# Performance work log

Hardware: AMD Instinct MI355X
Metric: run time of the kernel (lower is better)

## Reference

```python
import jax, jax.numpy as jnp
import numpy as np

SCALES = [2 ** i for i in range(11)]  # scales=10 -> [1,2,4,...,1024]


def _linear_upsample(x, N):
    """torch F.interpolate(mode='linear', align_corners=False) along last axis.
    x: (B, C, pn) -> (B, C, N)."""
    pn = x.shape[-1]
    scale = pn / N
    coords = (jnp.arange(N, dtype=x.dtype) + 0.5) * scale - 0.5
    coords = jnp.clip(coords, 0.0, pn - 1)
    i0 = jnp.floor(coords).astype(jnp.int32)
    i1 = jnp.minimum(i0 + 1, pn - 1)
    w = (coords - i0.astype(x.dtype))
    return x[..., i0] * (1.0 - w) + x[..., i1] * w


def setup_inputs() -> dict:
    key = jax.random.key(0)
    k1, k2 = jax.random.split(key)
    B, N, C, K = 32, 1024, 512, 4096
    f_BNC = jax.random.normal(k1, (B, N, C), dtype=jnp.float32)
    # torch init: uniform(-1/K, 1/K)
    codebook = (jax.random.uniform(k2, (K, C), dtype=jnp.float32) * 2.0 - 1.0) / K
    return {"f_BNC": f_BNC, "codebook": codebook}


def reference(f_BNC, codebook):
    f_BCN = jnp.transpose(f_BNC, (0, 2, 1))  # (B, C, N)
    B, C, N = f_BCN.shape
    f_ng = jax.lax.stop_gradient(f_BCN)      # f_no_grad
    f_rest = f_ng
    f_hat = jnp.zeros_like(f_ng)
    Wd = jax.lax.stop_gradient(codebook)     # embedding.weight.data for distances
    w_sq = jnp.sum(Wd * Wd, axis=1)          # (K,)
    SN = len(SCALES)
    commit = jnp.zeros((), dtype=f_BCN.dtype)
    qlat = jnp.zeros((), dtype=f_BCN.dtype)
    for pn in SCALES:
        # area downsample: exact block mean since N % pn == 0
        r = f_rest.reshape(B, C, pn, N // pn).mean(axis=-1)        # (B, C, pn)
        z = jnp.transpose(r, (0, 2, 1)).reshape(B * pn, C)          # (B*pn, C)
        d = jnp.sum(z * z, axis=1, keepdims=True) + w_sq - 2.0 * (z @ Wd.T)  # (B*pn, K)
        p = jax.nn.softmax(d, axis=-1)
        h = (p @ codebook).reshape(B, pn, C)                        # soft codebook lookup
        h = jnp.transpose(h, (0, 2, 1))                             # (B, C, pn)
        h = _linear_upsample(h, N)                                  # (B, C, N)
        f_hat = f_hat + h
        f_rest = f_rest - h
        commit = commit + 0.25 * jnp.mean((jax.lax.stop_gradient(f_hat) - f_BCN) ** 2)
        qlat = qlat + jnp.mean((f_hat - f_ng) ** 2)
    commit = commit / SN
    qlat = qlat / SN
    # straight-through estimator
    f_hat_st = jax.lax.stop_gradient(f_hat) - f_ng + f_BCN
    return jnp.transpose(f_hat_st, (0, 2, 1)), commit, qlat
```

## Files before the change

### kernel.cpp

```cpp
#include <hip/hip_runtime.h>
#include <hip/hip_bf16.h>

constexpr int B = 32, N = 1024, C = 512, K = 4096, SN = 11;
constexpr long BCN = (long)B * N * C;
constexpr int TKC = 128;
constexpr int NCH = K / TKC;
constexpr float PSCALE = 256.f;
constexpr int SCONE = 0x7f7f7f7f;

typedef __attribute__((ext_vector_type(4))) float f32x4;
typedef __attribute__((ext_vector_type(16))) float f32x16;
typedef __attribute__((ext_vector_type(8))) int i32x8;
typedef __attribute__((ext_vector_type(4))) int i32x4;
typedef unsigned int u32;
typedef unsigned long u64;

static __device__ __forceinline__ short f2bf(float x) {
  __hip_bfloat16 h = __float2bfloat16(x);
  short s;
  __builtin_memcpy(&s, &h, sizeof(s));
  return s;
}
static __device__ __forceinline__ float bf2f(short s) {
  u32 u = ((u32)(unsigned short)s) << 16;
  float f;
  __builtin_memcpy(&f, &u, 4);
  return f;
}
static __device__ __forceinline__ u32 pk4_fp8(float a, float b, float c, float d) {
  int r = __builtin_amdgcn_cvt_pk_fp8_f32(a, b, 0, false);
  r = __builtin_amdgcn_cvt_pk_fp8_f32(c, d, r, true);
  return (u32)r;
}
static __device__ __forceinline__ f32x16 zero16() {
  f32x16 z;
#pragma unroll
  for (int i = 0; i < 16; ++i) z[i] = 0.f;
  return z;
}

__global__ __launch_bounds__(256) void wsq_kernel(const float* __restrict__ W,
                                                  float* __restrict__ wsq) {
  __shared__ float red[256];
  int k = blockIdx.x;
  const float* row = W + (long)k * C;
  float s = 0.f;
  for (int c = threadIdx.x; c < C; c += 256) {
    float v = row[c];
    s += v * v;
  }
  red[threadIdx.x] = s;
  __syncthreads();
  for (int off = 128; off > 0; off >>= 1) {
    if (threadIdx.x < off) red[threadIdx.x] += red[threadIdx.x + off];
    __syncthreads();
  }
  if (threadIdx.x == 0) wsq[k] = red[0];
}

__global__ __launch_bounds__(256) void colsum_kernel(const float* __restrict__ W,
                                                     float* __restrict__ csum) {
  int ch = blockIdx.x;
  const float* base = W + (long)ch * TKC * C;
  float s0 = 0.f, s1 = 0.f;
  for (int k = 0; k < TKC; ++k) {
    s0 += base[(long)k * C + threadIdx.x];
    s1 += base[(long)k * C + threadIdx.x + 256];
  }
  csum[ch * C + threadIdx.x] = s0;
  csum[ch * C + threadIdx.x + 256] = s1;
}

__global__ __launch_bounds__(256) void prep_w(const float* __restrict__ W,
                                              unsigned char* __restrict__ WnA,
                                              unsigned char* __restrict__ WtB) {
  __shared__ __attribute__((aligned(16))) unsigned char tile[32 * 520];
  const int blk = blockIdx.x, tid = threadIdx.x;
  const float* src = W + (long)blk * 32 * C;
#pragma unroll
  for (int i = 0; i < 16; ++i) {
    int idx = tid + i * 256;
    float4 v = ((const float4*)src)[idx];
    int key = idx >> 7, c = (idx & 127) * 4;
    *(u32*)&tile[key * 520 + c] = pk4_fp8(v.x, v.y, v.z, v.w);
  }
  __syncthreads();
#pragma unroll
  for (int i = 0; i < 2; ++i) {
    int slot = tid + i * 256;
    int cc = slot >> 6, L = slot & 63;
    const unsigned char* sp = &tile[(L & 31) * 520 + cc * 64 + (L >> 5) * 32];
    u64* dst = (u64*)(WnA + ((long)(blk * 8 + cc) * 64 + L) * 32);
    dst[0] = *(const u64*)(sp);
    dst[1] = *(const u64*)(sp + 8);
    dst[2] = *(const u64*)(sp + 16);
    dst[3] = *(const u64*)(sp + 24);
  }
#pragma unroll
  for (int i = 0; i < 2; ++i) {
    int slot = tid + i * 256;
    int c2 = slot >> 5, rho = slot & 31;
    union { unsigned char v[32]; u64 q[4]; } t;
#pragma unroll
    for (int j = 0; j < 32; ++j) t.v[j] = tile[j * 520 + c2 * 32 + rho];
    u64* dst = (u64*)(WtB + ((long)((blk >> 1) * 16 + c2) * 64 + (blk & 1) * 32 + rho) * 32);
    dst[0] = t.q[0]; dst[1] = t.q[1]; dst[2] = t.q[2]; dst[3] = t.q[3];
  }
}

__global__ __launch_bounds__(256) void init_f(const float* __restrict__ f,
                                              short* __restrict__ fbf,
                                              float* __restrict__ zpart) {
  int b = blockIdx.x >> 5;
  int n0 = (blockIdx.x & 31) * 32 + (threadIdx.x >> 7) * 16;
  int c4 = threadIdx.x & 127;
  float ax = 0, ay = 0, az = 0, aw = 0;
  for (int j = 0; j < 16; ++j) {
    long e = ((long)b * N + n0 + j) * 128 + c4;
    float4 v = ((const float4*)f)[e];
    short4 o = {f2bf(v.x), f2bf(v.y), f2bf(v.z), f2bf(v.w)};
    ((short4*)fbf)[e] = o;
    ax += v.x; ay += v.y; az += v.z; aw += v.w;
  }
  float4 zp = {ax, ay, az, aw};
  ((float4*)zpart)[((long)b * 64 + (n0 >> 4)) * 128 + c4] = zp;
}

__global__ __launch_bounds__(256) void reduce_zpart(const float* __restrict__ zpart,
                                                    unsigned char* __restrict__ zq, int pn) {
  long idx = (long)blockIdx.x * 256 + threadIdx.x;
  long tot = (long)B * pn * 128;
  if (idx >= tot) return;
  int c4 = (int)(idx & 127);
  long row = idx >> 7;
  int b = (int)(row / pn), j = (int)(row % pn);
  int r = 64 / pn;
  float ax = 0, ay = 0, az = 0, aw = 0;
  for (int i = 0; i < r; ++i) {
    float4 v = ((const float4*)zpart)[((long)b * 64 + j * r + i) * 128 + c4];
    ax += v.x; ay += v.y; az += v.z; aw += v.w;
  }
  float inv = (float)pn / (float)N;
  *(u32*)&zq[row * C + c4 * 4] = pk4_fp8(ax * inv, ay * inv, az * inv, aw * inv);
}

__global__ __launch_bounds__(256, 2) void flash_mfma(
    const unsigned char* __restrict__ zq, const unsigned char* __restrict__ WnA,
    const unsigned char* __restrict__ WtB, const float* __restrict__ wsq,
    const float* __restrict__ csum, short* __restrict__ hb,
    float* __restrict__ lpart, int M, int KS) {
  __shared__ __attribute__((aligned(16))) unsigned char ZS[16 * 2048];
  __shared__ __attribute__((aligned(16))) unsigned char PS[2][4 * 2048];
  const int tid = threadIdx.x;
  const int w = tid >> 6, lane = tid & 63;
  const int rho = lane & 31, hi = lane >> 5;
  const long row0 = (long)blockIdx.x * 64;
  const int nc = NCH / KS, ch0 = blockIdx.y * nc;

#pragma unroll
  for (int i = 0; i < 4; ++i) {
    int u = i * 4 + w, zt = u >> 3, cc = u & 7;
    long row = row0 + zt * 32 + rho;
    u64 v0 = 0, v1 = 0, v2 = 0, v3 = 0;
    if (row < M) {
      const u64* sp = (const u64*)(zq + row * C + cc * 64 + hi * 32);
      v0 = sp[0]; v1 = sp[1]; v2 = sp[2]; v3 = sp[3];
    }
    u64* dp = (u64*)(ZS + u * 2048 + lane * 32);
    dp[0] = v0; dp[1] = v1; dp[2] = v2; dp[3] = v3;
  }
  f32x16 hacc[2][4];
#pragma unroll
  for (int zt = 0; zt < 2; ++zt)
#pragma unroll
    for (int ct = 0; ct < 4; ++ct) hacc[zt][ct] = zero16();
  float lreg[2] = {0.f, 0.f};
  float cs[4] = {0.f, 0.f, 0.f, 0.f};
  __syncthreads();

#pragma unroll 1
  for (int ci = 0; ci < nc; ++ci) {
    const int ch = ch0 + ci;
#pragma unroll
    for (int ct = 0; ct < 4; ++ct) cs[ct] += csum[ch * C + w * 128 + ct * 32 + rho];
    f32x16 s[2];
    s[0] = zero16();
    s[1] = zero16();
    const unsigned char* wa = WnA + ((long)(ch * 4 + w) * 8) * 2048 + lane * 32;
    const unsigned char* zb = ZS + lane * 32;
#pragma unroll
    for (int cc = 0; cc < 8; ++cc) {
      i32x8 a = *(const i32x8*)(wa + cc * 2048);
      i32x8 b0 = *(const i32x8*)(zb + cc * 2048);
      i32x8 b1 = *(const i32x8*)(zb + (8 + cc) * 2048);
      s[0] = __builtin_amdgcn_mfma_scale_f32_32x32x64_f8f6f4(a, b0, s[0], 0, 0, 0, SCONE, 0, SCONE);
      s[1] = __builtin_amdgcn_mfma_scale_f32_32x32x64_f8f6f4(a, b1, s[1], 0, 0, 0, SCONE, 0, SCONE);
    }
    const float* wsb = wsq + ch * TKC + w * 32 + hi * 4;
    float wv[16];
#pragma unroll
    for (int g = 0; g < 4; ++g) {
      float4 t = *(const float4*)(wsb + 8 * g);
      wv[4 * g + 0] = t.x; wv[4 * g + 1] = t.y; wv[4 * g + 2] = t.z; wv[4 * g + 3] = t.w;
    }
    unsigned char* Pun = PS[ci & 1] + (w >> 1) * 2048;
    const int pbase = (w & 1) * 1024 + rho * 32 + hi * 4;
#pragma unroll
    for (int zt = 0; zt < 2; ++zt) {
      float sum = 0.f, pv[16];
#pragma unroll
      for (int r = 0; r < 16; ++r) {
        float e = __expf(wv[r] - 2.f * s[zt][r]);
        sum += e;
        pv[r] = PSCALE * e - PSCALE;
      }
      lreg[zt] += sum;
#pragma unroll
      for (int g = 0; g < 4; ++g) {
        u32 pk = pk4_fp8(pv[4 * g], pv[4 * g + 1], pv[4 * g + 2], pv[4 * g + 3]);
        *(u32*)(Pun + zt * 4096 + pbase + 8 * g) = pk;
      }
    }
    __syncthreads();
#pragma unroll
    for (int kc = 0; kc < 2; ++kc) {
      const unsigned char* Pr = PS[ci & 1] + lane * 32;
      i32x8 pa[2];
      pa[0] = *(const i32x8*)(Pr + (0 * 2 + kc) * 2048);
      pa[1] = *(const i32x8*)(Pr + (1 * 2 + kc) * 2048);
      const unsigned char* wb = WtB + ((long)(ch * 2) * 16 + w * 4) * 2048 + lane * 32;
#pragma unroll
      for (int ct = 0; ct < 4; ++ct) {
        i32x8 bw = *(const i32x8*)(wb + (kc * 16 + ct) * 2048);
        hacc[0][ct] = __builtin_amdgcn_mfma_scale_f32_32x32x64_f8f6f4(pa[0], bw, hacc[0][ct], 0, 0, 0, SCONE, 0, SCONE);
        hacc[1][ct] = __builtin_amdgcn_mfma_scale_f32_32x32x64_f8f6f4(pa[1], bw, hacc[1][ct], 0, 0, 0, SCONE, 0, SCONE);
      }
    }
  }
  __syncthreads();
  lreg[0] += __shfl_xor(lreg[0], 32);
  lreg[1] += __shfl_xor(lreg[1], 32);
  float* l4 = (float*)PS;
  if (hi == 0) {
    l4[rho * 4 + w] = lreg[0];
    l4[(32 + rho) * 4 + w] = lreg[1];
  }
  __syncthreads();
  constexpr float PINV = 1.f / PSCALE;
  if (KS == 1) {
#pragma unroll
    for (int zt = 0; zt < 2; ++zt)
#pragma unroll
      for (int r = 0; r < 16; ++r) {
        int rr = zt * 32 + (r & 3) + 8 * (r >> 2) + 4 * hi;
        long row = row0 + rr;
        if (row < M) {
          float4 lv = ((const float4*)l4)[rr];
          float inv = 1.f / (lv.x + lv.y + lv.z + lv.w);
#pragma unroll
          for (int ct = 0; ct < 4; ++ct)
            hb[row * C + (w * 4 + ct) * 32 + rho] =
                f2bf((cs[ct] + hacc[zt][ct][r] * PINV) * inv);
        }
      }
  } else {
    long base = (long)blockIdx.y * M * C;
#pragma unroll
    for (int zt = 0; zt < 2; ++zt)
#pragma unroll
      for (int r = 0; r < 16; ++r) {
        int rr = zt * 32 + (r & 3) + 8 * (r >> 2) + 4 * hi;
        long row = row0 + rr;
        if (row < M) {
#pragma unroll
          for (int ct = 0; ct < 4; ++ct)
            hb[base + row * C + (w * 4 + ct) * 32 + rho] =
                f2bf(cs[ct] + hacc[zt][ct][r] * PINV);
        }
      }
    if (w == 0) {
      long row = row0 + lane;
      if (row < M) {
        float4 lv = ((const float4*)l4)[lane];
        lpart[(long)blockIdx.y * M + row] = lv.x + lv.y + lv.z + lv.w;
      }
    }
  }
}

__global__ __launch_bounds__(256) void combine_kernel(short* __restrict__ hb,
                                                      const float* __restrict__ lpart,
                                                      int M, int KS) {
  long idx = (long)blockIdx.x * 256 + threadIdx.x;
  long tot = (long)M * 128;
  if (idx >= tot) return;
  int m = (int)(idx >> 7);
  float lsum = 0.f;
  for (int s = 0; s < KS; ++s) lsum += lpart[(long)s * M + m];
  float ax = 0, ay = 0, az = 0, aw = 0;
  for (int s = 0; s < KS; ++s) {
    short4 v = ((const short4*)hb)[(long)s * tot + idx];
    ax += bf2f(v.x); ay += bf2f(v.y); az += bf2f(v.z); aw += bf2f(v.w);
  }
  float inv = 1.f / lsum;
  short4 o = {f2bf(ax * inv), f2bf(ay * inv), f2bf(az * inv), f2bf(aw * inv)};
  ((short4*)hb)[idx] = o;
}

__global__ __launch_bounds__(256) void fused_up(
    const short* __restrict__ hb, const short* __restrict__ fbf,
    const short* fhin, short* fhout, float* __restrict__ outf,
    unsigned char* __restrict__ zq, float* __restrict__ zpart,
    double* __restrict__ accum, int pn, int pn_next, int first, int last) {
  const int b = blockIdx.x >> 5;
  const int n0 = (blockIdx.x & 31) * 32 + (threadIdx.x >> 7) * 16;
  const int c4 = threadIdx.x & 127;
  const float scale = (float)pn * (1.f / (float)N);
  const int bs_next = pn_next ? (N / pn_next) : 0;
  float zx = 0, zy = 0, zz = 0, zw = 0, part = 0.f;
  for (int j = 0; j < 16; ++j) {
    int n = n0 + j;
    long e = ((long)b * N + n) * 128 + c4;
    float coords = ((float)n + 0.5f) * scale - 0.5f;
    coords = fminf(fmaxf(coords, 0.f), (float)(pn - 1));
    int i0 = (int)coords;
    int i1 = min(i0 + 1, pn - 1);
    float wq = coords - (float)i0, ow = 1.f - wq;
    short4 h0 = ((const short4*)hb)[((long)b * pn + i0) * 128 + c4];
    short4 h1 = ((const short4*)hb)[((long)b * pn + i1) * 128 + c4];
    short4 fv = ((const short4*)fbf)[e];
    float fhx, fhy, fhz, fhw;
    if (first) {
      fhx = fhy = fhz = fhw = 0.f;
    } else {
      short4 p = ((const short4*)fhin)[e];
      fhx = bf2f(p.x); fhy = bf2f(p.y); fhz = bf2f(p.z); fhw = bf2f(p.w);
    }
    fhx += bf2f(h0.x) * ow + bf2f(h1.x) * wq;
    fhy += bf2f(h0.y) * ow + bf2f(h1.y) * wq;
    fhz += bf2f(h0.z) * ow + bf2f(h1.z) * wq;
    fhw += bf2f(h0.w) * ow + bf2f(h1.w) * wq;
    if (last) {
      float4 o = {fhx, fhy, fhz, fhw};
      ((float4*)outf)[e] = o;
    } else {
      short4 o = {f2bf(fhx), f2bf(fhy), f2bf(fhz), f2bf(fhw)};
      ((short4*)fhout)[e] = o;
    }
    float dx = fhx - bf2f(fv.x), dy = fhy - bf2f(fv.y);
    float dz = fhz - bf2f(fv.z), dw = fhw - bf2f(fv.w);
    part += dx * dx + dy * dy + dz * dz + dw * dw;
    zx -= dx; zy -= dy; zz -= dz; zw -= dw;
    if (pn_next >= 64) {
      if (((n + 1) & (bs_next - 1)) == 0) {
        float inv = 1.f / (float)bs_next;
        *(u32*)&zq[((long)b * pn_next + n / bs_next) * C + c4 * 4] =
            pk4_fp8(zx * inv, zy * inv, zz * inv, zw * inv);
        zx = zy = zz = zw = 0.f;
      }
    }
  }
  if (pn_next && pn_next < 64) {
    float4 zp = {zx, zy, zz, zw};
    ((float4*)zpart)[((long)b * 64 + (n0 >> 4)) * 128 + c4] = zp;
  }
  __shared__ float red[256];
  red[threadIdx.x] = part;
  __syncthreads();
  for (int off = 128; off > 0; off >>= 1) {
    if (threadIdx.x < off) red[threadIdx.x] += red[threadIdx.x + off];
    __syncthreads();
  }
  if (threadIdx.x == 0) atomicAdd(&accum[blockIdx.x & 255], (double)red[0]);
}

__global__ void finalize_kernel(const double* __restrict__ accum,
                                float* __restrict__ out_scalars) {
  if (threadIdx.x == 0 && blockIdx.x == 0) {
    double s = 0.0;
    for (int i = 0; i < 256; ++i) s += accum[i];
    double denom = (double)SN * (double)BCN;
    out_scalars[0] = (float)(0.25 * s / denom);
    out_scalars[1] = (float)(s / denom);
  }
}

extern "C" void kernel_launch(void* const* d_in, const int* in_sizes, int n_in,
                              void* d_out, int out_size, void* d_ws, size_t ws_size,
                              hipStream_t stream) {
  const float* f = (const float*)d_in[0];
  const float* W = (const float*)d_in[1];
  float* out = (float*)d_out;

  const long MBy = 1l << 20;
  char* ws = (char*)d_ws;
  short* hb = (short*)ws;
  short* fbf = (short*)(ws + 32 * MBy);
  short* fhbf = (short*)(ws + 64 * MBy);
  unsigned char* zq = (unsigned char*)(ws + 96 * MBy);
  unsigned char* WnA = (unsigned char*)(ws + 112 * MBy);
  unsigned char* WtB = (unsigned char*)(ws + 114 * MBy);
  float* zpart = (float*)(ws + 116 * MBy);
  float* wsqf = (float*)(ws + 120 * MBy);
  float* csum = (float*)(ws + 120 * MBy + (1l << 16));
  float* lpart = (float*)(ws + 120 * MBy + (1l << 17));
  double* accum = (double*)(ws + 121 * MBy);

  hipMemsetAsync(accum, 0, 256 * sizeof(double), stream);

  wsq_kernel<<<K, 256, 0, stream>>>(W, wsqf);
  colsum_kernel<<<NCH, 256, 0, stream>>>(W, csum);
  prep_w<<<K / 32, 256, 0, stream>>>(W, WnA, WtB);
  init_f<<<B * 32, 256, 0, stream>>>(f, fbf, zpart);
  reduce_zpart<<<(B * 128 + 255) / 256, 256, 0, stream>>>(zpart, zq, 1);

  for (int s = 0; s < SN; ++s) {
    int pn = 1 << s;
    int M = B * pn;
    int gx = (M + 63) / 64;
    int KS = 512 / gx;
    if (KS < 1) KS = 1;
    if (KS > 32) KS = 32;
    flash_mfma<<<dim3(gx, KS), 256, 0, stream>>>(zq, WnA, WtB, wsqf, csum, hb, lpart, M, KS);
    if (KS > 1)
      combine_kernel<<<(int)(((long)M * 128 + 255) / 256), 256, 0, stream>>>(hb, lpart, M, KS);
    int pn_next = (s < SN - 1) ? (pn << 1) : 0;
    fused_up<<<B * 32, 256, 0, stream>>>(hb, fbf, fhbf, fhbf, out, zq, zpart, accum,
                                         pn, pn_next, s == 0 ? 1 : 0, s == SN - 1 ? 1 : 0);
    if (pn_next && pn_next < 64)
      reduce_zpart<<<(int)(((long)B * pn_next * 128 + 255) / 256), 256, 0, stream>>>(zpart, zq, pn_next);
  }

  finalize_kernel<<<1, 64, 0, stream>>>(accum, out + BCN);
}
```

Baseline: 951.9 us.

## Fuse split-K combine into upsample kernel and fold exp scaling into exp2

Removes the separate combine_kernel by having fused_up reduce the KS partial h rows and softmax denominators on the fly, caching the two interpolation source rows per thread. The softmax exponent switches to exp2, with log2e and the PSCALE factor folded into the precomputed wsq bias, and the row sums are rescaled afterwards. This cuts launches and a round-trip of hb through memory. The trade-off is redundant partial reductions across blocks sharing the same batch.

```diff
diff --git a/kernel.cpp b/kernel.cpp
--- a/kernel.cpp
+++ b/kernel.cpp
@@ -7,6 +7,7 @@
 constexpr int NCH = K / TKC;
 constexpr float PSCALE = 256.f;
 constexpr int SCONE = 0x7f7f7f7f;
+constexpr float LOG2E = 1.4426950408889634f;
 
 typedef __attribute__((ext_vector_type(4))) float f32x4;
 typedef __attribute__((ext_vector_type(16))) float f32x16;
@@ -55,7 +56,7 @@
     if (threadIdx.x < off) red[threadIdx.x] += red[threadIdx.x + off];
     __syncthreads();
   }
-  if (threadIdx.x == 0) wsq[k] = red[0];
+  if (threadIdx.x == 0) wsq[k] = red[0] * LOG2E + 8.0f;
 }
 
 __global__ __launch_bounds__(256) void colsum_kernel(const float* __restrict__ W,
@@ -156,6 +157,7 @@
   const int rho = lane & 31, hi = lane >> 5;
   const long row0 = (long)blockIdx.x * 64;
   const int nc = NCH / KS, ch0 = blockIdx.y * nc;
+  constexpr float NL2E = -2.f * LOG2E;
 
 #pragma unroll
   for (int i = 0; i < 4; ++i) {
@@ -210,9 +212,9 @@
       float sum = 0.f, pv[16];
 #pragma unroll
       for (int r = 0; r < 16; ++r) {
-        float e = __expf(wv[r] - 2.f * s[zt][r]);
-        sum += e;
-        pv[r] = PSCALE * e - PSCALE;
+        float e8 = __builtin_amdgcn_exp2f(fmaf(s[zt][r], NL2E, wv[r]));
+        sum += e8;
+        pv[r] = e8 - PSCALE;
       }
       lreg[zt] += sum;
 #pragma unroll
@@ -240,6 +242,8 @@
   __syncthreads();
   lreg[0] += __shfl_xor(lreg[0], 32);
   lreg[1] += __shfl_xor(lreg[1], 32);
+  lreg[0] *= 0.00390625f;
+  lreg[1] *= 0.00390625f;
   float* l4 = (float*)PS;
   if (hi == 0) {
     l4[rho * 4 + w] = lreg[0];
@@ -288,36 +292,32 @@
   }
 }
 
-__global__ __launch_bounds__(256) void combine_kernel(short* __restrict__ hb,
-                                                      const float* __restrict__ lpart,
-                                                      int M, int KS) {
-  long idx = (long)blockIdx.x * 256 + threadIdx.x;
-  long tot = (long)M * 128;
-  if (idx >= tot) return;
-  int m = (int)(idx >> 7);
-  float lsum = 0.f;
-  for (int s = 0; s < KS; ++s) lsum += lpart[(long)s * M + m];
-  float ax = 0, ay = 0, az = 0, aw = 0;
-  for (int s = 0; s < KS; ++s) {
-    short4 v = ((const short4*)hb)[(long)s * tot + idx];
-    ax += bf2f(v.x); ay += bf2f(v.y); az += bf2f(v.z); aw += bf2f(v.w);
-  }
-  float inv = 1.f / lsum;
-  short4 o = {f2bf(ax * inv), f2bf(ay * inv), f2bf(az * inv), f2bf(aw * inv)};
-  ((short4*)hb)[idx] = o;
-}
-
 __global__ __launch_bounds__(256) void fused_up(
-    const short* __restrict__ hb, const short* __restrict__ fbf,
-    const short* fhin, short* fhout, float* __restrict__ outf,
-    unsigned char* __restrict__ zq, float* __restrict__ zpart,
-    double* __restrict__ accum, int pn, int pn_next, int first, int last) {
+    const short* __restrict__ hb, const float* __restrict__ lpart,
+    const short* __restrict__ fbf, const short* fhin, short* fhout,
+    float* __restrict__ outf, unsigned char* __restrict__ zq,
+    float* __restrict__ zpart, double* __restrict__ accum,
+    int pn, int pn_next, int KS, int first, int last) {
   const int b = blockIdx.x >> 5;
   const int n0 = (blockIdx.x & 31) * 32 + (threadIdx.x >> 7) * 16;
   const int c4 = threadIdx.x & 127;
+  const int M = B * pn;
   const float scale = (float)pn * (1.f / (float)N);
   const int bs_next = pn_next ? (N / pn_next) : 0;
   float zx = 0, zy = 0, zz = 0, zw = 0, part = 0.f;
+  int cache_i0 = -1, cache_i1 = -1;
+  float4 ch0 = {0, 0, 0, 0}, ch1 = {0, 0, 0, 0};
+  auto comb = [&](int row) -> float4 {
+    long m = (long)b * pn + row;
+    float ls = 0.f, ax = 0.f, ay = 0.f, az = 0.f, aw = 0.f;
+    for (int s2 = 0; s2 < KS; ++s2) {
+      ls += lpart[(long)s2 * M + m];
+      short4 v = ((const short4*)hb)[(long)s2 * M * 128 + m * 128 + c4];
+      ax += bf2f(v.x); ay += bf2f(v.y); az += bf2f(v.z); aw += bf2f(v.w);
+    }
+    float iv = 1.f / ls;
+    return (float4){ax * iv, ay * iv, az * iv, aw * iv};
+  };
   for (int j = 0; j < 16; ++j) {
     int n = n0 + j;
     long e = ((long)b * N + n) * 128 + c4;
@@ -326,8 +326,24 @@
     int i0 = (int)coords;
     int i1 = min(i0 + 1, pn - 1);
     float wq = coords - (float)i0, ow = 1.f - wq;
-    short4 h0 = ((const short4*)hb)[((long)b * pn + i0) * 128 + c4];
-    short4 h1 = ((const short4*)hb)[((long)b * pn + i1) * 128 + c4];
+    float4 hh0, hh1;
+    if (KS == 1) {
+      short4 h0 = ((const short4*)hb)[((long)b * pn + i0) * 128 + c4];
+      short4 h1 = ((const short4*)hb)[((long)b * pn + i1) * 128 + c4];
+      hh0 = (float4){bf2f(h0.x), bf2f(h0.y), bf2f(h0.z), bf2f(h0.w)};
+      hh1 = (float4){bf2f(h1.x), bf2f(h1.y), bf2f(h1.z), bf2f(h1.w)};
+    } else {
+      if (i0 != cache_i0) {
+        ch0 = (i0 == cache_i1) ? ch1 : comb(i0);
+        cache_i0 = i0;
+      }
+      if (i1 != cache_i1) {
+        ch1 = (i1 == i0) ? ch0 : comb(i1);
+        cache_i1 = i1;
+      }
+      hh0 = ch0;
+      hh1 = ch1;
+    }
     short4 fv = ((const short4*)fbf)[e];
     float fhx, fhy, fhz, fhw;
     if (first) {
@@ -336,10 +352,10 @@
       short4 p = ((const short4*)fhin)[e];
       fhx = bf2f(p.x); fhy = bf2f(p.y); fhz = bf2f(p.z); fhw = bf2f(p.w);
     }
-    fhx += bf2f(h0.x) * ow + bf2f(h1.x) * wq;
-    fhy += bf2f(h0.y) * ow + bf2f(h1.y) * wq;
-    fhz += bf2f(h0.z) * ow + bf2f(h1.z) * wq;
-    fhw += bf2f(h0.w) * ow + bf2f(h1.w) * wq;
+    fhx += hh0.x * ow + hh1.x * wq;
+    fhy += hh0.y * ow + hh1.y * wq;
+    fhz += hh0.z * ow + hh1.z * wq;
+    fhw += hh0.w * ow + hh1.w * wq;
     if (last) {
       float4 o = {fhx, fhy, fhz, fhw};
       ((float4*)outf)[e] = o;
@@ -422,11 +438,9 @@
     if (KS < 1) KS = 1;
     if (KS > 32) KS = 32;
     flash_mfma<<<dim3(gx, KS), 256, 0, stream>>>(zq, WnA, WtB, wsqf, csum, hb, lpart, M, KS);
-    if (KS > 1)
-      combine_kernel<<<(int)(((long)M * 128 + 255) / 256), 256, 0, stream>>>(hb, lpart, M, KS);
     int pn_next = (s < SN - 1) ? (pn << 1) : 0;
-    fused_up<<<B * 32, 256, 0, stream>>>(hb, fbf, fhbf, fhbf, out, zq, zpart, accum,
-                                         pn, pn_next, s == 0 ? 1 : 0, s == SN - 1 ? 1 : 0);
+    fused_up<<<B * 32, 256, 0, stream>>>(hb, lpart, fbf, fhbf, fhbf, out, zq, zpart, accum,
+                                         pn, pn_next, KS, s == 0 ? 1 : 0, s == SN - 1 ? 1 : 0);
     if (pn_next && pn_next < 64)
       reduce_zpart<<<(int)(((long)B * pn_next * 128 + 255) / 256), 256, 0, stream>>>(zpart, zq, pn_next);
   }
```

After: 919.4 us. 1.04x faster.
